# Optimization experiments

Measured on AMD Instinct MI355X. Metric: run time of the kernel, lower is better.

Reference implementation:

```python
import jax, jax.numpy as jnp
from jax import lax
import numpy as np

ALPHA = 1.0
GAMMA = 1e-6
KBLK = 64  # codebook block size for the L1 NN search scan


def setup_inputs() -> dict:
    key = jax.random.key(0)
    ks = jax.random.split(key, 6)
    B, T, C, F, D, K = 8, 1024, 32, 256, 128, 512
    return {
        "X": jax.random.normal(ks[0], (B, T, C), jnp.float32),
        "H": jax.random.normal(ks[1], (B, D, T), jnp.float32),
        "M": jax.random.normal(ks[2], (D, K), jnp.float32),
        "Hdec": jax.random.normal(ks[3], (B, T, F), jnp.float32),
        "W": jax.random.normal(ks[4], (C, F), jnp.float32) * 0.05,
        "w_d": jax.random.normal(ks[5], (C,), jnp.float32) * 0.05,
    }


def _memory_loss(H, M):
    # H: [B, D, T], M: [D, K]
    Ht = jnp.transpose(H, (0, 2, 1))            # [B, T, D]
    MT = M.T                                     # [K, D] codewords
    K, D = MT.shape
    nblk = K // KBLK
    blocks = MT.reshape(nblk, KBLK, D)
    bases = jnp.arange(nblk, dtype=jnp.int32) * KBLK

    def step(carry, blk_base):
        best_d, best_i = carry
        blk, base = blk_base
        # L1 distance to this block of codewords: [B, T, KBLK]
        d = jnp.sum(jnp.abs(Ht[:, :, None, :] - blk[None, None, :, :]), axis=-1)
        bd = jnp.min(d, axis=-1)
        bi = jnp.argmin(d, axis=-1).astype(jnp.int32) + base
        upd = bd < best_d  # strict < keeps the first (lowest-index) argmin, as torch does
        return (jnp.where(upd, bd, best_d), jnp.where(upd, bi, best_i)), None

    init = (jnp.full(Ht.shape[:2], jnp.inf, Ht.dtype),
            jnp.zeros(Ht.shape[:2], jnp.int32))
    (_, best_i), _ = lax.scan(step, init, (blocks, bases))

    Zt = MT[best_i]  # [B, T, D] gathered nearest codewords
    sg = lax.stop_gradient
    # sum of per-(b,d) squared L2 norms over T == total squared sum
    diffs = jnp.sum((sg(Ht) - Zt) ** 2) + jnp.sum((Ht - sg(Zt)) ** 2)
    return diffs / float(np.prod(H.shape))


def reference(X, H, M, Hdec, W, w_d):
    # decoder last layer + discriminator head (needed for adaptive weight grads)
    def rec_loss(w):
        Xhat = jnp.einsum('btf,cf->btc', Hdec, w)
        return jnp.mean((Xhat - X) ** 2)

    def d_loss(w):
        Xhat = jnp.einsum('btf,cf->btc', Hdec, w)
        return -jnp.mean(Xhat @ w_d)

    loss_rec = rec_loss(W)
    loss_d = d_loss(W)
    loss_m = _memory_loss(H, M)

    g_rec = jax.grad(rec_loss)(W)
    g_d = jax.grad(d_loss)(W)
    lmbda = lax.stop_gradient(
        jnp.linalg.norm(g_rec) / (jnp.linalg.norm(g_d) + GAMMA))

    return loss_rec + ALPHA * loss_m + lmbda * loss_d
```

## Files before the change

kernel.cpp:

```cpp
#include <hip/hip_runtime.h>
#include <hip/hip_bf16.h>
#include <math.h>

#define N_POS 8192
#define D_DIM 128
#define K_DIM 512
#define C_DIM 32
#define F_DIM 256
#define NKT   4
#define GREC_COLS 8448
#define L2_BLOCKS 388
#define XG_BLOCKS 256
#define NN_BLOCKS 1024
#define GRID_L1   1280

__device__ __forceinline__ float block_reduce_256(float v) {
    __shared__ float sbuf[4];
    __syncthreads();
#pragma unroll
    for (int off = 32; off > 0; off >>= 1) v += __shfl_down(v, off);
    const int lane = threadIdx.x & 63;
    const int w    = threadIdx.x >> 6;
    if (lane == 0) sbuf[w] = v;
    __syncthreads();
    return (threadIdx.x == 0) ? (sbuf[0] + sbuf[1] + sbuf[2] + sbuf[3]) : 0.f;
}

__global__ __launch_bounds__(256, 6)
void fused_l1(const float* __restrict__ H, const float* __restrict__ M,
              const float* __restrict__ Hdec, const float* __restrict__ W,
              const float* __restrict__ X, const float* __restrict__ w_d,
              float* __restrict__ MT, float* __restrict__ pd,
              int* __restrict__ pi, float* __restrict__ pp,
              float* __restrict__ accum) {
    __shared__ __align__(16) float smem[5120];
    const int tid = threadIdx.x;

    if (blockIdx.x >= XG_BLOCKS) {
        float* hT = smem;
        float* mT = smem + 1024;
        float* rd = smem;
        int*   ri = (int*)(smem + 1024);

        const int nb    = blockIdx.x - XG_BLOCKS;
        const int ptile = nb >> 2;
        const int ktile = nb & 3;
        const int pos0  = ptile << 5;
        const int b     = pos0 >> 10;
        const int t0    = pos0 & 1023;
        const int k0    = ktile << 7;
        const float* Hb = H + (b << 17) + t0;

        const int hsr = tid >> 3;
        const int hsc = (tid & 7) << 2;
        const int msr = tid >> 5;
        const int msc = (tid & 31) << 2;
        const int p4  = (tid & 7) << 2;
        const int q4  = (tid >> 3) << 2;

        float acc[4][4];
#pragma unroll
        for (int i = 0; i < 4; ++i)
#pragma unroll
            for (int j = 0; j < 4; ++j) acc[i][j] = 0.f;

        for (int ch = 0; ch < 4; ++ch) {
            const int d0 = ch << 5;
            __syncthreads();
            *(float4*)(hT + (hsr << 5) + hsc) =
                *(const float4*)(Hb + ((size_t)(d0 + hsr) << 10) + hsc);
#pragma unroll
            for (int p = 0; p < 4; ++p) {
                const int d = (p << 3) + msr;
                *(float4*)(mT + (d << 7) + msc) =
                    *(const float4*)(M + (size_t)(d0 + d) * K_DIM + k0 + msc);
            }
            __syncthreads();

#pragma unroll 4
            for (int d = 0; d < 32; ++d) {
                const float4 ha = *(const float4*)(hT + (d << 5) + p4);
                const float4 ma = *(const float4*)(mT + (d << 7) + q4);
                const float hh[4] = {ha.x, ha.y, ha.z, ha.w};
                const float mm[4] = {ma.x, ma.y, ma.z, ma.w};
#pragma unroll
                for (int i = 0; i < 4; ++i)
#pragma unroll
                    for (int j = 0; j < 4; ++j) {
                        const float dv = hh[i] - mm[j];
                        asm("v_add_f32 %0, %0, abs(%1)"
                            : "+v"(acc[i][j]) : "v"(dv));
                    }
            }
        }

        __syncthreads();

        const int kg = tid >> 3;
#pragma unroll
        for (int i = 0; i < 4; ++i) {
            const int pl = p4 + i;
            float bd = acc[i][0];
            int   bj = 0;
#pragma unroll
            for (int j = 1; j < 4; ++j)
                if (acc[i][j] < bd) { bd = acc[i][j]; bj = j; }
            rd[kg * 32 + pl] = bd;
            ri[kg * 32 + pl] = k0 + q4 + bj;
        }
        __syncthreads();

        if (tid < 32) {
            float bd = rd[tid];
            int   bi = ri[tid];
#pragma unroll
            for (int q = 1; q < 32; ++q) {
                const float d = rd[q * 32 + tid];
                const int   k = ri[q * 32 + tid];
                if (d < bd || (d == bd && k < bi)) { bd = d; bi = k; }
            }
            pd[ktile * N_POS + pos0 + tid] = bd;
            pi[ktile * N_POS + pos0 + tid] = bi;
        }
    } else {
        float* El = smem;
        const int xb  = blockIdx.x;
        const int bt0 = xb << 5;

        if (xb < 64) {
            const int d0 = xb << 1;
            const int d  = d0 + (tid >> 7);
            const int k  = (tid & 127) << 2;
#pragma unroll
            for (int j = 0; j < 4; ++j)
                MT[(size_t)(k + j) * D_DIM + d] = M[(size_t)d * K_DIM + k + j];
        }

        const int c  = tid & 31;
        const int rg = tid >> 5;
        const int r0 = bt0 + rg, r1 = r0 + 8, r2 = r0 + 16, r3 = r0 + 24;

        const float* Wc = W + (size_t)c * F_DIM;

        float a0 = 0.f, a1 = 0.f, a2 = 0.f, a3 = 0.f;
#pragma unroll 4
        for (int f0 = 0; f0 < F_DIM; f0 += 4) {
            const float4 w4 = *(const float4*)(Wc + f0);
            const float4 h0 = *(const float4*)(Hdec + (size_t)r0 * F_DIM + f0);
            const float4 h1 = *(const float4*)(Hdec + (size_t)r1 * F_DIM + f0);
            const float4 h2 = *(const float4*)(Hdec + (size_t)r2 * F_DIM + f0);
            const float4 h3 = *(const float4*)(Hdec + (size_t)r3 * F_DIM + f0);
            a0 += h0.x * w4.x + h0.y * w4.y + h0.z * w4.z + h0.w * w4.w;
            a1 += h1.x * w4.x + h1.y * w4.y + h1.z * w4.z + h1.w * w4.w;
            a2 += h2.x * w4.x + h2.y * w4.y + h2.z * w4.z + h2.w * w4.w;
            a3 += h3.x * w4.x + h3.y * w4.y + h3.z * w4.z + h3.w * w4.w;
        }

        const float wd = w_d[c];
        const float e0 = a0 - X[(size_t)r0 * C_DIM + c];
        const float e1 = a1 - X[(size_t)r1 * C_DIM + c];
        const float e2 = a2 - X[(size_t)r2 * C_DIM + c];
        const float e3 = a3 - X[(size_t)r3 * C_DIM + c];
        El[(rg)      * 32 + c] = e0;
        El[(rg + 8)  * 32 + c] = e1;
        El[(rg + 16) * 32 + c] = e2;
        El[(rg + 24) * 32 + c] = e3;
        const float sse = e0 * e0 + e1 * e1 + e2 * e2 + e3 * e3;
        const float dp  = (a0 + a1 + a2 + a3) * wd;
        const float rA = block_reduce_256(sse);
        if (tid == 0) atomicAdd(accum + 0, rA);
        const float rB = block_reduce_256(dp);
        if (tid == 0) atomicAdd(accum + 1, rB);
        __syncthreads();

        const int f = tid;
        const float* hp = Hdec + (size_t)bt0 * F_DIM + f;
        float gacc[C_DIM];
#pragma unroll
        for (int cc = 0; cc < C_DIM; ++cc) gacc[cc] = 0.f;
        float sf = 0.f;
        float hd0 = hp[0];
        float hd1 = hp[F_DIM];
#pragma unroll 1
        for (int i = 0; i < 30; ++i) {
            const float hdn = hp[(size_t)(i + 2) * F_DIM];
            sf += hd0;
#pragma unroll
            for (int c4 = 0; c4 < 8; ++c4) {
                const float4 e4 = *(const float4*)(El + i * 32 + c4 * 4);
                gacc[c4 * 4 + 0] += e4.x * hd0;
                gacc[c4 * 4 + 1] += e4.y * hd0;
                gacc[c4 * 4 + 2] += e4.z * hd0;
                gacc[c4 * 4 + 3] += e4.w * hd0;
            }
            hd0 = hd1; hd1 = hdn;
        }
#pragma unroll
        for (int i = 30; i < 32; ++i) {
            sf += hd0;
#pragma unroll
            for (int c4 = 0; c4 < 8; ++c4) {
                const float4 e4 = *(const float4*)(El + i * 32 + c4 * 4);
                gacc[c4 * 4 + 0] += e4.x * hd0;
                gacc[c4 * 4 + 1] += e4.y * hd0;
                gacc[c4 * 4 + 2] += e4.z * hd0;
                gacc[c4 * 4 + 3] += e4.w * hd0;
            }
            hd0 = hd1;
        }
        float* o = pp + (size_t)xb * GREC_COLS;
#pragma unroll
        for (int cc = 0; cc < C_DIM; ++cc) o[cc * F_DIM + f] = gacc[cc];
        o[8192 + f] = sf;
    }
}

__global__ __launch_bounds__(256)
void fused_l2(const float* __restrict__ H, const float* __restrict__ MT,
              const float* __restrict__ pd, const int* __restrict__ pi,
              const float* __restrict__ pp, const float* __restrict__ w_d,
              float* __restrict__ accum, float* __restrict__ out) {
    const int tid = threadIdx.x;
    if (blockIdx.x < 256) {
        const int bx = blockIdx.x & 31;
        const int by = blockIdx.x >> 5;
        const int pos = bx * 256 + tid;
        const int b = pos >> 10;
        const int t = pos & 1023;

        const int d0 = by * 16;
        const float* Hb = H + (b << 17) + t + (d0 << 10);
        float hv[16];
#pragma unroll
        for (int j = 0; j < 16; ++j) hv[j] = Hb[j << 10];

        float bd = INFINITY;
        int   bi = 0x7fffffff;
#pragma unroll
        for (int p = 0; p < NKT; ++p) {
            const float d = pd[p * N_POS + pos];
            const int   k = pi[p * N_POS + pos];
            if (d < bd || (d == bd && k < bi)) { bd = d; bi = k; }
        }

        const float* z  = MT + (size_t)bi * D_DIM + d0;
        const float4 z0 = *(const float4*)(z);
        const float4 z1 = *(const float4*)(z + 4);
        const float4 z2 = *(const float4*)(z + 8);
        const float4 z3 = *(const float4*)(z + 12);
        float s0 = 0.f, s1 = 0.f, s2 = 0.f, s3 = 0.f;
        float e;
        e = hv[0]  - z0.x; s0 += e * e;
        e = hv[1]  - z0.y; s1 += e * e;
        e = hv[2]  - z0.z; s2 += e * e;
        e = hv[3]  - z0.w; s3 += e * e;
        e = hv[4]  - z1.x; s0 += e * e;
        e = hv[5]  - z1.y; s1 += e * e;
        e = hv[6]  - z1.z; s2 += e * e;
        e = hv[7]  - z1.w; s3 += e * e;
        e = hv[8]  - z2.x; s0 += e * e;
        e = hv[9]  - z2.y; s1 += e * e;
        e = hv[10] - z2.z; s2 += e * e;
        e = hv[11] - z2.w; s3 += e * e;
        e = hv[12] - z3.x; s0 += e * e;
        e = hv[13] - z3.y; s1 += e * e;
        e = hv[14] - z3.z; s2 += e * e;
        e = hv[15] - z3.w; s3 += e * e;
        const float r = block_reduce_256((s0 + s1) + (s2 + s3));
        if (tid == 0) atomicAdd(accum + 2, r);
    } else {
        const int g = blockIdx.x - 256;
        const int col = (g < 128) ? (g * 64 + (tid & 63))
                                  : (8192 + (g - 128) * 64 + (tid & 63));
        const int pc  = tid >> 6;
        const float* base = pp + (size_t)(pc * 64) * GREC_COLS + col;
        float s = 0.f;
#pragma unroll 8
        for (int p = 0; p < 64; ++p) s += base[(size_t)p * GREC_COLS];
        __shared__ float red[4][64];
        red[pc][tid & 63] = s;
        __syncthreads();
        if (tid < 64) {
            const float tot = red[0][tid] + red[1][tid] +
                              red[2][tid] + red[3][tid];
            float v = tot * tot;
#pragma unroll
            for (int off = 32; off > 0; off >>= 1) v += __shfl_down(v, off);
            if (tid == 0)
                atomicAdd(accum + ((g >= 128) ? 4 : 3), v);
        }
    }

    __shared__ int is_last;
    if (tid == 0) {
        __threadfence();
        unsigned int* cnt = (unsigned int*)(accum + 5);
        is_last = (atomicAdd(cnt, 1u) == L2_BLOCKS - 1);
    }
    __syncthreads();
    if (is_last && tid < 64) {
        float wd2 = (tid < C_DIM) ? w_d[tid] * w_d[tid] : 0.f;
#pragma unroll
        for (int off = 32; off > 0; off >>= 1) wd2 += __shfl_down(wd2, off);
        if (tid == 0) {
            __threadfence();
            const float sse_rec = atomicAdd(accum + 0, 0.f);
            const float dsum    = atomicAdd(accum + 1, 0.f);
            const float sse_mem = atomicAdd(accum + 2, 0.f);
            const float g2      = atomicAdd(accum + 3, 0.f);
            const float s2      = atomicAdd(accum + 4, 0.f);
            const float loss_rec = sse_rec / 262144.f;
            const float loss_d   = -dsum / 8192.f;
            const float loss_m   = 2.f * sse_mem / 1048576.f;
            const float ngrec    = (2.f / 262144.f) * sqrtf(g2);
            const float ngd      = sqrtf(wd2 * s2) / 8192.f;
            const float lmbda    = ngrec / (ngd + 1e-6f);
            out[0] = loss_rec + loss_m + lmbda * loss_d;
        }
    }
}

extern "C" void kernel_launch(void* const* d_in, const int* in_sizes, int n_in,
                              void* d_out, int out_size, void* d_ws, size_t ws_size,
                              hipStream_t stream) {
    const float* X    = (const float*)d_in[0];
    const float* H    = (const float*)d_in[1];
    const float* M    = (const float*)d_in[2];
    const float* Hdec = (const float*)d_in[3];
    const float* W    = (const float*)d_in[4];
    const float* w_d  = (const float*)d_in[5];

    float* ws    = (float*)d_ws;
    float* MT    = ws;
    float* accum = ws + 65536;
    float* pd    = ws + 65552;
    int*   pi    = (int*)(ws + 98320);
    float* pp    = ws + 131088;

    hipMemsetAsync(accum, 0, 16 * sizeof(float), stream);
    fused_l1<<<GRID_L1,   256, 0, stream>>>(H, M, Hdec, W, X, w_d,
                                            MT, pd, pi, pp, accum);
    fused_l2<<<L2_BLOCKS, 256, 0, stream>>>(H, MT, pd, pi, pp, w_d,
                                            accum, (float*)d_out);
}
```

Before: 124.5 us.

## Double-buffer L1 distance tiles with async global-to-LDS loads

Staging of the H and M chunks in the L1 nearest-neighbour search now uses global_load_lds direct copies into two LDS buffers. The next chunk is prefetched while the current one is computed, which removes the register round-trip and one barrier per chunk. In exchange, shared memory doubles to 40 KB per block and the launch bound drops from 6 to 4 waves. That may lower occupancy, and correctness depends on the barrier waiting for the async LDS writes.

```diff
diff --git a/kernel.cpp b/kernel.cpp
--- a/kernel.cpp
+++ b/kernel.cpp
@@ -14,6 +14,12 @@
 #define NN_BLOCKS 1024
 #define GRID_L1   1280
 
+__device__ __forceinline__ void gll16(const float* g, float* l) {
+    __builtin_amdgcn_global_load_lds(
+        (const __attribute__((address_space(1))) void*)g,
+        (__attribute__((address_space(3))) void*)l, 16, 0, 0);
+}
+
 __device__ __forceinline__ float block_reduce_256(float v) {
     __shared__ float sbuf[4];
     __syncthreads();
@@ -26,19 +32,19 @@
     return (threadIdx.x == 0) ? (sbuf[0] + sbuf[1] + sbuf[2] + sbuf[3]) : 0.f;
 }
 
-__global__ __launch_bounds__(256, 6)
+__global__ __launch_bounds__(256, 4)
 void fused_l1(const float* __restrict__ H, const float* __restrict__ M,
               const float* __restrict__ Hdec, const float* __restrict__ W,
               const float* __restrict__ X, const float* __restrict__ w_d,
               float* __restrict__ MT, float* __restrict__ pd,
               int* __restrict__ pi, float* __restrict__ pp,
               float* __restrict__ accum) {
-    __shared__ __align__(16) float smem[5120];
+    __shared__ __align__(16) float smem[10240];
     const int tid = threadIdx.x;
 
     if (blockIdx.x >= XG_BLOCKS) {
         float* hT = smem;
-        float* mT = smem + 1024;
+        float* mT = smem + 2048;
         float* rd = smem;
         int*   ri = (int*)(smem + 1024);
 
@@ -51,12 +57,14 @@
         const int k0    = ktile << 7;
         const float* Hb = H + (b << 17) + t0;
 
-        const int hsr = tid >> 3;
-        const int hsc = (tid & 7) << 2;
-        const int msr = tid >> 5;
-        const int msc = (tid & 31) << 2;
-        const int p4  = (tid & 7) << 2;
-        const int q4  = (tid >> 3) << 2;
+        const int wv = tid >> 6;
+        const int p4 = (tid & 7) << 2;
+        const int q4 = (tid >> 3) << 2;
+
+        const float* hsrc = Hb + (size_t)(tid >> 3) * 1024 + ((tid & 7) << 2);
+        const float* msrc = M + (size_t)(tid >> 5) * K_DIM + k0 + ((tid & 31) << 2);
+        float* hdstw = hT + (wv << 8);
+        float* mdstw = mT + (wv << 8);
 
         float acc[4][4];
 #pragma unroll
@@ -64,23 +72,29 @@
 #pragma unroll
             for (int j = 0; j < 4; ++j) acc[i][j] = 0.f;
 
+        gll16(hsrc, hdstw);
+#pragma unroll
+        for (int p = 0; p < 4; ++p)
+            gll16(msrc + (size_t)(p << 3) * K_DIM, mdstw + (p << 10));
+
         for (int ch = 0; ch < 4; ++ch) {
-            const int d0 = ch << 5;
             __syncthreads();
-            *(float4*)(hT + (hsr << 5) + hsc) =
-                *(const float4*)(Hb + ((size_t)(d0 + hsr) << 10) + hsc);
-#pragma unroll
-            for (int p = 0; p < 4; ++p) {
-                const int d = (p << 3) + msr;
-                *(float4*)(mT + (d << 7) + msc) =
-                    *(const float4*)(M + (size_t)(d0 + d) * K_DIM + k0 + msc);
-            }
-            __syncthreads();
-
+            if (ch < 3) {
+                const int nd0  = (ch + 1) << 5;
+                const int nsel = (ch + 1) & 1;
+                gll16(hsrc + ((size_t)nd0 << 10), hdstw + (nsel << 10));
+#pragma unroll
+                for (int p = 0; p < 4; ++p)
+                    gll16(msrc + (size_t)(nd0 + (p << 3)) * K_DIM,
+                          mdstw + (nsel << 12) + (p << 10));
+            }
+
+            const float* hc = hT + ((ch & 1) << 10);
+            const float* mc = mT + ((ch & 1) << 12);
 #pragma unroll 4
             for (int d = 0; d < 32; ++d) {
-                const float4 ha = *(const float4*)(hT + (d << 5) + p4);
-                const float4 ma = *(const float4*)(mT + (d << 7) + q4);
+                const float4 ha = *(const float4*)(hc + (d << 5) + p4);
+                const float4 ma = *(const float4*)(mc + (d << 7) + q4);
                 const float hh[4] = {ha.x, ha.y, ha.z, ha.w};
                 const float mm[4] = {ma.x, ma.y, ma.z, ma.w};
 #pragma unroll
```

Result: slower. 129.9 us (+4.3%).
